# Performance work log

Hardware: AMD Instinct MI355X
Metric: run time of the kernel (lower is better)

Reference implementation:

```python
import jax, jax.numpy as jnp
import numpy as np

NUM_HEADS = 8

def _spline_scores(x):
    # x: (BH, S, E), softmax-normalized. Kernel per pair (i,j):
    #   sum_{e,f} [ max*min + 0.5*min^2*max - min^3/6 ] + E^2
    # using min*max = a*b  =>  a*b*(1 + 0.5*min) - min^3/6
    E = x.shape[-1]
    xi = x[:, :, None, :, None]          # (BH, S, 1, E, 1)
    xj = x[:, None, :, None, :]          # (BH, 1, S, 1, E)
    m = jnp.minimum(xi, xj)              # (BH, S, S, E, E)
    k = xi * xj * (1.0 + 0.5 * m) - (m * m * m) * (1.0 / 6.0)
    return k.sum(axis=(-1, -2)) + jnp.asarray(E * E, x.dtype)  # (BH, S, S)

def setup_inputs() -> dict:
    key = jax.random.key(0)
    k1, k2, k3 = jax.random.split(key, 3)
    B, S, D = 2, 128, 256
    scale = 1.0 / np.sqrt(D)
    return {
        "inputs": jax.random.normal(k1, (B, S, D), dtype=jnp.float32),
        "w_in": jax.random.normal(k2, (D, D), dtype=jnp.float32) * scale,
        "b_in": jnp.zeros((D,), dtype=jnp.float32),
        "w_out": jax.random.normal(k3, (D, D), dtype=jnp.float32) * scale,
        "b_out": jnp.zeros((D,), dtype=jnp.float32),
    }

def reference(inputs, w_in, b_in, w_out, b_out):
    B, S, D = inputs.shape
    H = NUM_HEADS
    E = D // H
    x = jnp.einsum('bsd,ed->bse', inputs, w_in) + b_in          # in_project (torch Linear: x @ W.T + b)
    x = x.reshape(B, S, H, E).transpose(0, 2, 1, 3).reshape(B * H, S, E)
    x = jax.nn.softmax(x, axis=-1)
    attn = _spline_scores(x) / E                                 # (BH, S, S)
    attn = jax.nn.softmax(attn, axis=-1)                         # dropout is identity at inference
    out = jnp.einsum('bij,bje->bie', attn, x)                    # (BH, S, E)
    out = out.reshape(B, H, S, E).transpose(0, 2, 1, 3).reshape(B, S, D)
    return jnp.einsum('bsd,ed->bse', out, w_out) + b_out
```

## Files before the change

kernel.cpp:

```cpp
#include <hip/hip_runtime.h>
#include <math.h>

constexpr int BB = 2;
constexpr int SS = 128;
constexpr int DD = 256;
constexpr int HH = 8;
constexpr int EE = 32;

__global__ __launch_bounds__(256) void spline_k1(
    const float* __restrict__ inp,
    const float* __restrict__ w_in,
    const float* __restrict__ b_in,
    float* __restrict__ xs_out)
{
  const int row = blockIdx.x;
  const int e = threadIdx.x;
  __shared__ float in_row[DD];
  __shared__ float vals[DD];
  __shared__ float exps[DD];

  in_row[e] = inp[row * DD + e];
  __syncthreads();

  const float* wr = w_in + e * DD;
  float acc = b_in[e];
#pragma unroll 8
  for (int d = 0; d < DD; d += 4) {
    const float4 w4 = *reinterpret_cast<const float4*>(wr + d);
    acc = fmaf(in_row[d + 0], w4.x, acc);
    acc = fmaf(in_row[d + 1], w4.y, acc);
    acc = fmaf(in_row[d + 2], w4.z, acc);
    acc = fmaf(in_row[d + 3], w4.w, acc);
  }
  vals[e] = acc;
  __syncthreads();

  const int h = e >> 5;
  const int base = h * EE;
  float mx = -1e30f;
#pragma unroll
  for (int k = 0; k < EE; ++k) mx = fmaxf(mx, vals[base + k]);
  const float ex = __expf(acc - mx);
  exps[e] = ex;
  __syncthreads();
  float sum = 0.f;
#pragma unroll
  for (int k = 0; k < EE; ++k) sum += exps[base + k];
  const float x = ex / sum;

  const int b = row / SS, s = row - b * SS;
  const int ee = e & 31;
  xs_out[(((b * HH + h) * SS) + s) * EE + ee] = x;
}

__global__ __launch_bounds__(128) void spline_k2(
    const float* __restrict__ xs_g,
    float* __restrict__ y)
{
  const int bh = blockIdx.x >> 7;
  const int i = blockIdx.x & 127;
  const int t = threadIdx.x;

  __shared__ float xs[SS * EE];
  __shared__ float sc[SS];
  __shared__ float at[SS];

  const float* src = xs_g + bh * SS * EE;
  for (int idx = t; idx < SS * EE; idx += 128) xs[idx] = src[idx];
  __syncthreads();

  float vrow[EE];
  float sv = 0.f;
#pragma unroll
  for (int k = 0; k < EE; ++k) {
    vrow[k] = xs[t * EE + ((k + t) & 31)];
    sv += vrow[k];
  }

  float acc = 0.f;
  float su = 0.f;
  for (int e1 = 0; e1 < EE; ++e1) {
    const float u = xs[i * EE + e1];
    su += u;
#pragma unroll
    for (int e2 = 0; e2 < EE; ++e2) {
      const float v = vrow[e2];
      const float m = fminf(u, v);
      const float p = u * v;
      const float m2 = m * m;
      const float s = fmaf(0.5f, p, m2 * (-1.0f / 6.0f));
      acc = fmaf(m, s, acc);
    }
  }
  const float logit = (fmaf(su, sv, acc) + (float)(EE * EE)) * (1.0f / (float)EE);

  sc[t] = logit;
  __syncthreads();
  float mx = -1e30f;
  for (int j = 0; j < SS; ++j) mx = fmaxf(mx, sc[j]);
  at[t] = __expf(logit - mx);
  __syncthreads();
  float sum = 0.f;
  for (int j = 0; j < SS; ++j) sum += at[j];

  if (t < EE) {
    float o = 0.f;
    for (int j = 0; j < SS; ++j) o = fmaf(at[j], xs[j * EE + t], o);
    o /= sum;
    const int b = bh >> 3, h = bh & 7;
    y[(b * SS + i) * DD + h * EE + t] = o;
  }
}

__global__ __launch_bounds__(256) void spline_k3(
    const float* __restrict__ y,
    const float* __restrict__ w_out,
    const float* __restrict__ b_out,
    float* __restrict__ out)
{
  const int row = blockIdx.x;
  const int e = threadIdx.x;
  __shared__ float yr[DD];
  yr[e] = y[row * DD + e];
  __syncthreads();

  const float* wr = w_out + e * DD;
  float acc = b_out[e];
#pragma unroll 8
  for (int d = 0; d < DD; d += 4) {
    const float4 w4 = *reinterpret_cast<const float4*>(wr + d);
    acc = fmaf(yr[d + 0], w4.x, acc);
    acc = fmaf(yr[d + 1], w4.y, acc);
    acc = fmaf(yr[d + 2], w4.z, acc);
    acc = fmaf(yr[d + 3], w4.w, acc);
  }
  out[row * DD + e] = acc;
}

extern "C" void kernel_launch(void* const* d_in, const int* in_sizes, int n_in,
                              void* d_out, int out_size, void* d_ws, size_t ws_size,
                              hipStream_t stream) {
  const float* inp   = (const float*)d_in[0];
  const float* w_in  = (const float*)d_in[1];
  const float* b_in  = (const float*)d_in[2];
  const float* w_out = (const float*)d_in[3];
  const float* b_out = (const float*)d_in[4];
  float* out = (float*)d_out;

  float* ws1 = (float*)d_ws;
  float* ws2 = ws1 + BB * HH * SS * EE;

  spline_k1<<<BB * SS, 256, 0, stream>>>(inp, w_in, b_in, ws1);
  spline_k2<<<BB * HH * SS, 128, 0, stream>>>(ws1, ws2);
  spline_k3<<<BB * SS, 256, 0, stream>>>(ws2, w_out, b_out, out);
}
```

Measured before the change: 108.5 us.

## Exploit score symmetry: split score and softmax kernels, compute upper triangle only

Splits the fused attention kernel into a score kernel and a softmax/AV kernel. The score kernel relies on the pairwise spline kernel being symmetric, computes only the upper triangle with a wrap-around pairing so each block does 128 pairs, and writes each value to both (i,j) and (j,i). It also algebraically folds the per-term expression (a factor of 0.5 pulled out of the inner loop) and uses four accumulators for ILP. The cost is an extra launch plus a global round trip for the BH×S×S score matrix. The second kernel uses wave shuffles for the max and sum reductions and spreads the AV product over all 128 threads.

```diff
diff --git a/kernel.cpp b/kernel.cpp
--- a/kernel.cpp
+++ b/kernel.cpp
@@ -53,62 +53,119 @@
   xs_out[(((b * HH + h) * SS) + s) * EE + ee] = x;
 }
 
-__global__ __launch_bounds__(128) void spline_k2(
+__global__ __launch_bounds__(128) void spline_k2a(
+    const float* __restrict__ xs_g,
+    float* __restrict__ sc_g)
+{
+  const int p = blockIdx.x;
+  const int bh = blockIdx.y;
+  const int t = threadIdx.x;
+
+  __shared__ float xs[SS * EE];
+  const float4* s4 = (const float4*)(xs_g + bh * SS * EE);
+  float4* x4 = (float4*)xs;
+#pragma unroll
+  for (int k = 0; k < 8; ++k) x4[t + 128 * k] = s4[t + 128 * k];
+  __syncthreads();
+
+  int i, j;
+  bool active = true;
+  if (p == 0) { i = 0; j = t; }
+  else if (p == 64) {
+    if (t < 64) { i = 64; j = 64 + t; } else { i = 0; j = 0; active = false; }
+  } else {
+    if (t >= p) { i = p; j = t; }
+    else        { i = 128 - p; j = 128 - p + t; }
+  }
+
+  float vrow[EE];
+  float sv = 0.f;
+#pragma unroll
+  for (int k = 0; k < EE; ++k) {
+    vrow[k] = xs[j * EE + ((k + t) & 31)];
+    sv += vrow[k];
+  }
+
+  float a0 = 0.f, a1 = 0.f, a2 = 0.f, a3 = 0.f, su = 0.f;
+  const int ibase = i * EE;
+#pragma unroll 4
+  for (int e1 = 0; e1 < EE; ++e1) {
+    const float u = xs[ibase + e1];
+    su += u;
+#pragma unroll
+    for (int e2 = 0; e2 < EE; e2 += 4) {
+      { const float v = vrow[e2 + 0], m = fminf(u, v), pm = u * v, w = m * m;
+        const float q2 = fmaf(w, -(1.f / 3.f), pm); a0 = fmaf(m, q2, a0); }
+      { const float v = vrow[e2 + 1], m = fminf(u, v), pm = u * v, w = m * m;
+        const float q2 = fmaf(w, -(1.f / 3.f), pm); a1 = fmaf(m, q2, a1); }
+      { const float v = vrow[e2 + 2], m = fminf(u, v), pm = u * v, w = m * m;
+        const float q2 = fmaf(w, -(1.f / 3.f), pm); a2 = fmaf(m, q2, a2); }
+      { const float v = vrow[e2 + 3], m = fminf(u, v), pm = u * v, w = m * m;
+        const float q2 = fmaf(w, -(1.f / 3.f), pm); a3 = fmaf(m, q2, a3); }
+    }
+  }
+  const float mins = 0.5f * ((a0 + a1) + (a2 + a3));
+  const float logit = (fmaf(su, sv, mins) + (float)(EE * EE)) * (1.0f / (float)EE);
+
+  if (active) {
+    float* base = sc_g + bh * SS * SS;
+    base[i * SS + j] = logit;
+    if (i != j) base[j * SS + i] = logit;
+  }
+}
+
+__global__ __launch_bounds__(128) void spline_k2b(
+    const float* __restrict__ sc_g,
     const float* __restrict__ xs_g,
     float* __restrict__ y)
 {
-  const int bh = blockIdx.x >> 7;
-  const int i = blockIdx.x & 127;
+  const int i = blockIdx.x;
+  const int bh = blockIdx.y;
   const int t = threadIdx.x;
 
   __shared__ float xs[SS * EE];
-  __shared__ float sc[SS];
   __shared__ float at[SS];
-
-  const float* src = xs_g + bh * SS * EE;
-  for (int idx = t; idx < SS * EE; idx += 128) xs[idx] = src[idx];
-  __syncthreads();
-
-  float vrow[EE];
-  float sv = 0.f;
-#pragma unroll
-  for (int k = 0; k < EE; ++k) {
-    vrow[k] = xs[t * EE + ((k + t) & 31)];
-    sv += vrow[k];
-  }
-
-  float acc = 0.f;
-  float su = 0.f;
-  for (int e1 = 0; e1 < EE; ++e1) {
-    const float u = xs[i * EE + e1];
-    su += u;
-#pragma unroll
-    for (int e2 = 0; e2 < EE; ++e2) {
-      const float v = vrow[e2];
-      const float m = fminf(u, v);
-      const float p = u * v;
-      const float m2 = m * m;
-      const float s = fmaf(0.5f, p, m2 * (-1.0f / 6.0f));
-      acc = fmaf(m, s, acc);
-    }
-  }
-  const float logit = (fmaf(su, sv, acc) + (float)(EE * EE)) * (1.0f / (float)EE);
-
-  sc[t] = logit;
-  __syncthreads();
-  float mx = -1e30f;
-  for (int j = 0; j < SS; ++j) mx = fmaxf(mx, sc[j]);
-  at[t] = __expf(logit - mx);
-  __syncthreads();
-  float sum = 0.f;
-  for (int j = 0; j < SS; ++j) sum += at[j];
-
-  if (t < EE) {
-    float o = 0.f;
-    for (int j = 0; j < SS; ++j) o = fmaf(at[j], xs[j * EE + t], o);
-    o /= sum;
+  __shared__ float part[128];
+  __shared__ float wred[4];
+
+  const float4* s4 = (const float4*)(xs_g + bh * SS * EE);
+  float4* x4 = (float4*)xs;
+#pragma unroll
+  for (int k = 0; k < 8; ++k) x4[t + 128 * k] = s4[t + 128 * k];
+
+  const float logit = sc_g[(bh * SS + i) * SS + t];
+
+  float mx = logit;
+#pragma unroll
+  for (int off = 32; off; off >>= 1) mx = fmaxf(mx, __shfl_xor(mx, off));
+  const int wid = t >> 6;
+  if ((t & 63) == 0) wred[wid] = mx;
+  __syncthreads();
+  mx = fmaxf(wred[0], wred[1]);
+
+  const float ex = __expf(logit - mx);
+  float sm = ex;
+#pragma unroll
+  for (int off = 32; off; off >>= 1) sm += __shfl_xor(sm, off);
+  __syncthreads();
+  if ((t & 63) == 0) wred[2 + wid] = sm;
+  at[t] = ex;
+  __syncthreads();
+  const float rs = 1.0f / (wred[2] + wred[3]);
+
+  const int e = t & 31, q = t >> 5;
+  float o = 0.f;
+#pragma unroll
+  for (int jj = 0; jj < 32; ++jj) {
+    const int j = q * 32 + jj;
+    o = fmaf(at[j], xs[j * EE + e], o);
+  }
+  part[t] = o;
+  __syncthreads();
+  if (t < 32) {
+    const float oo = (part[t] + part[t + 32] + part[t + 64] + part[t + 96]) * rs;
     const int b = bh >> 3, h = bh & 7;
-    y[(b * SS + i) * DD + h * EE + t] = o;
+    y[(b * SS + i) * DD + h * EE + t] = oo;
   }
 }
 
@@ -147,10 +204,12 @@
   const float* b_out = (const float*)d_in[4];
   float* out = (float*)d_out;
 
-  float* ws1 = (float*)d_ws;
-  float* ws2 = ws1 + BB * HH * SS * EE;
-
-  spline_k1<<<BB * SS, 256, 0, stream>>>(inp, w_in, b_in, ws1);
-  spline_k2<<<BB * HH * SS, 128, 0, stream>>>(ws1, ws2);
-  spline_k3<<<BB * SS, 256, 0, stream>>>(ws2, w_out, b_out, out);
-}
+  float* ws_x  = (float*)d_ws;
+  float* ws_sc = ws_x + BB * HH * SS * EE;
+  float* ws_y  = ws_sc + BB * HH * SS * SS;
+
+  spline_k1<<<BB * SS, 256, 0, stream>>>(inp, w_in, b_in, ws_x);
+  spline_k2a<<<dim3(65, BB * HH), 128, 0, stream>>>(ws_x, ws_sc);
+  spline_k2b<<<dim3(SS, BB * HH), 128, 0, stream>>>(ws_sc, ws_x, ws_y);
+  spline_k3<<<BB * SS, 256, 0, stream>>>(ws_y, w_out, b_out, out);
+}
```

After: 103.4 us. -4.7%, faster.
